# Optimization experiments

Measured on AMD Instinct MI355X. Metric: run time of the kernel, lower is better.

## Reference

```python
import jax, jax.numpy as jnp
import numpy as np
import math

# Config constants (match init_kwargs)
E = 8          # n_experts
TOPK = 2       # attn_topk
DIM = 1024     # transformer_dim
B = 4          # batch_size
S = 1024       # max_seq_len
H = 1024       # num_heads * head_dim
SCALE = 1.0 / math.sqrt(DIM)  # original divides scores by sqrt(self.dim)


def setup_inputs() -> dict:
    key = jax.random.key(0)
    ks = jax.random.split(key, 8)
    w = 0.02  # weight init scale
    return {
        "X": jax.random.normal(ks[0], (B, S, DIM), jnp.float32),
        "mask": jnp.ones((B, S), jnp.float32),
        "switch_W": jax.random.normal(ks[1], (DIM * S, E), jnp.float32) * w,
        "switch_b": jnp.zeros((E,), jnp.float32),
        "Wq": jax.random.normal(ks[2], (E, DIM, H), jnp.float32) * w,
        "bq": jnp.zeros((E, H), jnp.float32),
        "Wk": jax.random.normal(ks[3], (E, DIM, H), jnp.float32) * w,
        "bk": jnp.zeros((E, H), jnp.float32),
        "Wv": jax.random.normal(ks[4], (E, DIM, H), jnp.float32) * w,
        "bv": jnp.zeros((E, H), jnp.float32),
        "Wff": jax.random.normal(ks[5], (E, H, DIM), jnp.float32) * w,
        "bff": jnp.zeros((E, DIM), jnp.float32),
    }


def _dispatch_mask(route_prob):
    # top-k expert routing per batch element -> hard {0,1} mask [B, E]
    _, idx = jax.lax.top_k(route_prob, TOPK)  # [B, TOPK]
    b = route_prob.shape[0]
    return jnp.zeros((b, E), route_prob.dtype).at[jnp.arange(b)[:, None], idx].set(1.0)


def reference(X, mask, switch_W, switch_b, Wq, bq, Wk, bk, Wv, bv, Wff, bff):
    b, s, d = X.shape
    # Router: Linear(dim*seq_len -> n_experts) + softmax; preprocess -> idx_list
    logits = X.reshape(b, -1) @ switch_W + switch_b          # [B, E]
    route_prob = jax.nn.softmax(logits, axis=-1)
    m = _dispatch_mask(route_prob)                            # [B, E] dispatch mask (idx_list)

    # Per-expert Q/K/V projections (ColumnParallelLinearWithMoE over routed batches)
    Q = jnp.einsum('bsd,edh->ebsh', X, Wq) + bq[:, None, None, :]  # [E,B,S,H]
    K = jnp.einsum('bsd,edh->ebsh', X, Wk) + bk[:, None, None, :]
    V = jnp.einsum('bsd,edh->ebsh', X, Wv) + bv[:, None, None, :]

    # RowParallelMatmulWithMoE: per-expert scores, softmax (dropout p=0)
    scores = jnp.einsum('ebsh,ebth->ebst', Q, K) * SCALE      # [E,B,S,S]
    P = jax.nn.softmax(scores, axis=-1)

    # index_add_ combine of per-expert attn maps (second preprocess reuses same routing)
    A = jnp.einsum('be,ebst->bst', m, P)                      # [B,S,S]

    # ColumnParallelMatmulWithMoE: attn @ V per expert
    ctx = jnp.einsum('bst,ebth->ebsh', A, V)                  # [E,B,S,H]

    # RowParallelLinearWithMoE output projection, then index_add_ combine
    out = jnp.einsum('ebsh,ehd->ebsd', ctx, Wff) + bff[:, None, None, :]
    y = jnp.einsum('be,ebsd->bsd', m, out)                    # [B,S,DIM]
    return y
```

## Files before the change

### kernel.cpp

```cpp
#include <hip/hip_runtime.h>
#include <math.h>

typedef unsigned short u16;
typedef __attribute__((ext_vector_type(8))) short bffrag;
typedef __attribute__((ext_vector_type(4))) float f32x4;
typedef __attribute__((ext_vector_type(4))) unsigned short us4;
typedef __attribute__((ext_vector_type(8))) unsigned short us8;

#define SCALE_QK (1.0f/32.0f)

__device__ __forceinline__ u16 f2bf(float f) {
    unsigned u = __builtin_bit_cast(unsigned, f);
    u += 0x7fffu + ((u >> 16) & 1u);
    return (u16)(u >> 16);
}
__device__ __forceinline__ float bf2f(u16 v) {
    unsigned u = ((unsigned)v) << 16;
    return __builtin_bit_cast(float, u);
}

__device__ __forceinline__ void gld16(const u16* g, u16* l) {
    __builtin_amdgcn_global_load_lds(
        (const __attribute__((address_space(1))) void*)g,
        (__attribute__((address_space(3))) void*)l, 16, 0, 0);
}

__global__ __launch_bounds__(256) void router_partial(const float* __restrict__ X,
                                                      const float* __restrict__ sW,
                                                      float* __restrict__ part) {
    float acc[32];
    #pragma unroll
    for (int a = 0; a < 32; ++a) acc[a] = 0.f;
    int tid = blockIdx.x * 256 + threadIdx.x;
    #pragma unroll
    for (int q = 0; q < 4; ++q) {
        int i = tid + q * 262144;
        float4 w0 = *(const float4*)(sW + (size_t)i * 8);
        float4 w1 = *(const float4*)(sW + (size_t)i * 8 + 4);
        #pragma unroll
        for (int b = 0; b < 4; ++b) {
            float x = X[((size_t)b << 20) + i];
            acc[b*8+0] += x * w0.x; acc[b*8+1] += x * w0.y;
            acc[b*8+2] += x * w0.z; acc[b*8+3] += x * w0.w;
            acc[b*8+4] += x * w1.x; acc[b*8+5] += x * w1.y;
            acc[b*8+6] += x * w1.z; acc[b*8+7] += x * w1.w;
        }
    }
    __shared__ float wsum[4][32];
    int lane = threadIdx.x & 63, wv = threadIdx.x >> 6;
    #pragma unroll
    for (int a = 0; a < 32; ++a) {
        float v = acc[a];
        #pragma unroll
        for (int off = 32; off; off >>= 1) v += __shfl_down(v, off, 64);
        if (lane == 0) wsum[wv][a] = v;
    }
    __syncthreads();
    int t = threadIdx.x;
    if (t < 32)
        part[(size_t)t * 1024 + blockIdx.x] = wsum[0][t] + wsum[1][t] + wsum[2][t] + wsum[3][t];
}

__global__ __launch_bounds__(256) void router_final(const float* __restrict__ part,
                                                    const float* __restrict__ sb,
                                                    int* __restrict__ sel_need) {
    __shared__ float ps[32][8];
    __shared__ float lg[32];
    int t = threadIdx.x, a = t >> 3, c = t & 7;
    {
        float s = 0.f;
        const float* p = part + (size_t)a * 1024 + c * 128;
        for (int i = 0; i < 128; ++i) s += p[i];
        ps[a][c] = s;
    }
    __syncthreads();
    if (t < 32) {
        float v = 0.f;
        #pragma unroll
        for (int j = 0; j < 8; ++j) v += ps[t][j];
        lg[t] = v + sb[t & 7];
    }
    __syncthreads();
    if (t < 4) {
        int base = t * 8;
        int e1 = 0; float v1 = lg[base];
        for (int e = 1; e < 8; ++e) { if (lg[base + e] > v1) { v1 = lg[base + e]; e1 = e; } }
        int e2 = -1; float v2 = -INFINITY;
        for (int e = 0; e < 8; ++e) {
            if (e == e1) continue;
            if (lg[base + e] > v2) { v2 = lg[base + e]; e2 = e; }
        }
        sel_need[t * 2] = e1; sel_need[t * 2 + 1] = e2;
    }
    __syncthreads();
    if (t < 8) {
        int need = 0;
        for (int j = 0; j < 8; ++j) need |= (sel_need[j] == t);
        sel_need[8 + t] = need;
    }
}

__global__ __launch_bounds__(256) void cvt_all(const float* __restrict__ Wq,
                                               const float* __restrict__ Wk,
                                               const float* __restrict__ Wff,
                                               const float* __restrict__ X,
                                               const float* __restrict__ Wv,
                                               const float* __restrict__ bv,
                                               const int* __restrict__ sel_need,
                                               u16* __restrict__ WqT, u16* __restrict__ WkT,
                                               u16* __restrict__ WffT,
                                               u16* __restrict__ Xb, u16* __restrict__ WvB,
                                               float* __restrict__ cpart) {
    int z = blockIdx.z;
    int R0 = blockIdx.y * 128, C0 = blockIdx.x * 128;
    int t = threadIdx.x;
    if (z < 24) {
        int type = z >> 3, e = z & 7;
        if (!sel_need[8 + e]) return;
        const float* src = (type == 0 ? Wq : type == 1 ? Wk : Wff) + ((size_t)e << 20);
        u16* dst = (type == 0 ? WqT : type == 1 ? WkT : WffT) + ((size_t)e << 20);
        __shared__ u16 lt[128 * 136];
        int c = t & 127;
        int rh = (t >> 7) * 4;
        #pragma unroll
        for (int it = 0; it < 16; ++it) {
            int r4 = it * 8 + rh;
            us4 o;
            #pragma unroll
            for (int j = 0; j < 4; ++j)
                o[j] = f2bf(src[(size_t)(R0 + r4 + j) * 1024 + C0 + c]);
            *(us4*)&lt[c * 136 + r4] = o;
        }
        __syncthreads();
        int dd = (t & 15) * 8;
        int hh = t >> 4;
        #pragma unroll
        for (int it = 0; it < 8; ++it) {
            int cr = it * 16 + hh;
            us8 o = *(const us8*)&lt[cr * 136 + dd];
            *(us8*)(dst + (size_t)(C0 + cr) * 1024 + R0 + dd) = o;
        }
    } else if (z < 36) {
        const float* src; u16* dst;
        if (z < 28) {
            int b = z - 24;
            src = X + ((size_t)b << 20);  dst = Xb + ((size_t)b << 20);
        } else {
            int e = z - 28;
            if (!sel_need[8 + e]) return;
            src = Wv + ((size_t)e << 20);  dst = WvB + ((size_t)e << 20);
        }
        int r = t >> 4;
        int c8 = (t & 15) * 8;
        #pragma unroll
        for (int it = 0; it < 8; ++it) {
            int row = R0 + it * 16 + r;
            const float* sp = src + (size_t)row * 1024 + C0 + c8;
            float4 a = *(const float4*)sp;
            float4 b2 = *(const float4*)(sp + 4);
            us8 o;
            o[0] = f2bf(a.x); o[1] = f2bf(a.y); o[2] = f2bf(a.z); o[3] = f2bf(a.w);
            o[4] = f2bf(b2.x); o[5] = f2bf(b2.y); o[6] = f2bf(b2.z); o[7] = f2bf(b2.w);
            *(us8*)(dst + (size_t)row * 1024 + C0 + c8) = o;
        }
    } else {
        int idx = ((z - 36) << 6) + (blockIdx.y << 3) + blockIdx.x;
        int e = idx >> 5;
        if (!sel_need[8 + e]) return;
        int r = idx & 31;
        int d = (r & 3) * 256 + t;
        int h0 = (r >> 2) * 128;
        const float* W = Wff + ((size_t)e << 20) + (size_t)h0 * 1024 + d;
        const float* bvp = bv + e * 1024 + h0;
        float s = 0.f;
        #pragma unroll 4
        for (int h = 0; h < 128; ++h) s += bvp[h] * W[(size_t)h * 1024];
        cpart[(e * 8 + (r >> 2)) * 1024 + d] = s;
    }
}

__device__ __forceinline__ void stage_half8(const u16* g, int ld, u16* ldst, int tid) {
    int r = tid >> 3;
    int j = ((tid ^ r) & 7) * 8;
    gld16(g + (size_t)r * ld + j, ldst + tid * 8);
    gld16(g + (size_t)(r + 64) * ld + j, ldst + 4096 + tid * 8);
}

template<int Q, bool LASTVM>
__device__ __forceinline__ void phase8(const u16* Ac, const bffrag (&bfr)[4][2],
                                       f32x4 (&acc)[8][4], int rb, int l15, int x0,
                                       const u16* sg, int sld, u16* sdst, int tid) {
    bffrag af[2][2];
    #pragma unroll
    for (int mm = 0; mm < 2; ++mm) {
        int r = (rb + Q * 32 + mm * 16 + l15) * 64;
        af[mm][0] = *(const bffrag*)(Ac + r + x0);
        af[mm][1] = *(const bffrag*)(Ac + r + (x0 ^ 32));
    }
    __builtin_amdgcn_sched_barrier(0);
    stage_half8(sg, sld, sdst, tid);
    __builtin_amdgcn_sched_barrier(0);
    __builtin_amdgcn_s_barrier();
    asm volatile("s_waitcnt lgkmcnt(0)" ::: "memory");
    __builtin_amdgcn_sched_barrier(0);
    __builtin_amdgcn_s_setprio(1);
    #pragma unroll
    for (int ks = 0; ks < 2; ++ks)
        #pragma unroll
        for (int mm = 0; mm < 2; ++mm)
            #pragma unroll
            for (int nn = 0; nn < 4; ++nn)
                acc[Q*2+mm][nn] = __builtin_amdgcn_mfma_f32_16x16x32_bf16(
                    af[mm][ks], bfr[nn][ks], acc[Q*2+mm][nn], 0, 0, 0);
    __builtin_amdgcn_s_setprio(0);
    __builtin_amdgcn_sched_barrier(0);
    if (LASTVM) asm volatile("s_waitcnt vmcnt(4)" ::: "memory");
    __builtin_amdgcn_s_barrier();
}

__device__ __forceinline__ void gemm8(const u16* __restrict__ A, int lda,
                                      const u16* __restrict__ B, int ldb,
                                      int K, int m0, int n0, f32x4 (&acc)[8][4]) {
    __shared__ u16 lds[65536];
    const int tid = threadIdx.x, l = tid & 63, wid = tid >> 6;
    const int wr = wid >> 2, wc = wid & 3;
    const int l15 = l & 15;
    const int rb = wr * 128;
    const int cb = wc * 64;
    const int x0 = (((l >> 4) ^ (l & 7)) * 8);
    const int nt = K >> 6;

    const u16* Ag = A + (size_t)m0 * lda;
    const u16* Bg = B + (size_t)n0 * ldb;

    stage_half8(Ag,                          lda, lds,                 tid);
    stage_half8(Ag + (size_t)128 * lda,      lda, lds + 8192,          tid);
    stage_half8(Bg,                          ldb, lds + 16384,         tid);
    stage_half8(Bg + (size_t)128 * ldb,      ldb, lds + 16384 + 8192,  tid);
    stage_half8(Bg + 64,                     ldb, lds + 32768 + 16384, tid);
    stage_half8(Bg + 64 + (size_t)128 * ldb, ldb, lds + 32768 + 16384 + 8192, tid);
    asm volatile("s_waitcnt vmcnt(4)" ::: "memory");
    __builtin_amdgcn_s_barrier();

    for (int t7 = 0; t7 < nt; ++t7) {
        const int cur = t7 & 1;
        u16* Ac = lds + cur * 32768;
        u16* Bc = Ac + 16384;
        u16* An = lds + (cur ^ 1) * 32768;
        const int ka = (t7 + 1 < nt ? t7 + 1 : nt - 1) << 6;
        const int kb = (t7 + 2 < nt ? t7 + 2 : nt - 1) << 6;
        const u16* sA0 = Ag + ka;
        const u16* sA1 = Ag + (size_t)128 * lda + ka;
        const u16* sB0 = Bg + kb;
        const u16* sB1 = Bg + (size_t)128 * ldb + kb;

        bffrag bfr[4][2];
        #pragma unroll
        for (int nn = 0; nn < 4; ++nn) {
            int r = (cb + nn * 16 + l15) * 64;
            bfr[nn][0] = *(const bffrag*)(Bc + r + x0);
            bfr[nn][1] = *(const bffrag*)(Bc + r + (x0 ^ 32));
        }
        phase8<0, false>(Ac, bfr, acc, rb, l15, x0, sA0, lda, An, tid);
        phase8<1, false>(Ac, bfr, acc, rb, l15, x0, sA1, lda, An + 8192, tid);
        phase8<2, false>(Ac, bfr, acc, rb, l15, x0, sB0, ldb, Bc, tid);
        phase8<3, true >(Ac, bfr, acc, rb, l15, x0, sB1, ldb, Bc + 8192, tid);
    }
}

__device__ __forceinline__ void zero8(f32x4 (&acc)[8][4]) {
    #pragma unroll
    for (int m = 0; m < 8; ++m)
        #pragma unroll
        for (int n = 0; n < 4; ++n)
            #pragma unroll
            for (int i = 0; i < 4; ++i) acc[m][n][i] = 0.f;
}

__device__ __forceinline__ void epi8_bf16(u16* __restrict__ C, int ldc, float scale,
                                          const f32x4 (&acc)[8][4],
                                          const float* __restrict__ biasN,
                                          int M0, int N0) {
    const int tid = threadIdx.x, l = tid & 63, wid = tid >> 6;
    const int wr = wid >> 2, wc = wid & 3;
    const int m0 = M0 + wr * 128, n0 = N0 + wc * 64;
    const int l15 = l & 15, l4 = (l >> 4) * 4;
    #pragma unroll
    for (int mt = 0; mt < 8; ++mt)
        #pragma unroll
        for (int nn = 0; nn < 4; ++nn) {
            int col = n0 + nn * 16 + l15;
            float bn = biasN ? biasN[col] : 0.f;
            #pragma unroll
            for (int i = 0; i < 4; ++i) {
                int row = m0 + mt * 16 + l4 + i;
                C[(size_t)row * ldc + col] = f2bf(acc[mt][nn][i] * scale + bn);
            }
        }
}

__device__ __forceinline__ void xcd_decode(int f, int& z, int& m0, int& n0) {
    int xcd = f & 7, slot = f >> 3;
    z = xcd + ((slot >> 4) << 3);
    int idx = slot & 15;
    m0 = (idx >> 2) * 256;
    n0 = (idx & 3) * 256;
}

__global__ __launch_bounds__(512) void mfma8_qk(const u16* __restrict__ Xb,
        const u16* __restrict__ WqT, const u16* __restrict__ WkT,
        const float* __restrict__ bq, const float* __restrict__ bk,
        const int* __restrict__ sel, u16* __restrict__ Qb, u16* __restrict__ Kb) {
    int z, m0, n0;
    xcd_decode(blockIdx.x, z, m0, n0);
    int w = z >> 3, bs = z & 7;
    int b = bs >> 1, e = sel[bs];
    f32x4 acc[8][4]; zero8(acc);
    gemm8(Xb + ((size_t)b << 20), 1024, (w ? WkT : WqT) + ((size_t)e << 20), 1024,
          1024, m0, n0, acc);
    epi8_bf16((w ? Kb : Qb) + ((size_t)bs << 20), 1024, 1.0f, acc,
              (w ? bk : bq) + e * 1024, m0, n0);
}

__global__ __launch_bounds__(512) void mfma8_sw(const u16* __restrict__ Qb,
        const u16* __restrict__ Kb, const u16* __restrict__ WffT,
        const u16* __restrict__ WvB, const int* __restrict__ sel,
        u16* __restrict__ Sb, u16* __restrict__ P0b, u16* __restrict__ P1b) {
    int z, m0, n0;
    xcd_decode(blockIdx.x, z, m0, n0);
    f32x4 acc[8][4]; zero8(acc);
    if (z < 8) {
        gemm8(Qb + ((size_t)z << 20), 1024, Kb + ((size_t)z << 20), 1024, 1024, m0, n0, acc);
        epi8_bf16(Sb + ((size_t)z << 20), 1024, SCALE_QK, acc, nullptr, m0, n0);
    } else {
        int h = (z >= 12), b = z & 3, e = sel[b * 2 + h];
        gemm8(WffT + ((size_t)e << 20), 1024, WvB + ((size_t)e << 20), 1024, 1024, m0, n0, acc);
        epi8_bf16((h ? P1b : P0b) + ((size_t)b << 20), 1024, 1.0f, acc, nullptr, m0, n0);
    }
}

__global__ __launch_bounds__(256) void wvfadd(const u16* __restrict__ P0b,
                                              const u16* __restrict__ P1b,
                                              u16* __restrict__ W,
                                              const float* __restrict__ cpart,
                                              const float* __restrict__ bff,
                                              const int* __restrict__ sel,
                                              float* __restrict__ ybias) {
    int bid = blockIdx.x;
    if (bid >= 2048) {
        int r = bid - 2048;
        int b = r >> 2;
        int d = (r & 3) * 256 + threadIdx.x;
        int e0 = sel[b * 2], e1 = sel[b * 2 + 1];
        float c0 = 0.f, c1v = 0.f;
        #pragma unroll
        for (int hc = 0; hc < 8; ++hc) {
            c0  += cpart[(e0 * 8 + hc) * 1024 + d];
            c1v += cpart[(e1 * 8 + hc) * 1024 + d];
        }
        ybias[b * 1024 + d] = 2.f * (c0 + c1v) + bff[e0 * 1024 + d] + bff[e1 * 1024 + d];
        return;
    }
    size_t i = (size_t)(bid * 256 + threadIdx.x) * 8;
    us8 a = *(const us8*)(P0b + i);
    us8 b = *(const us8*)(P1b + i);
    us8 o;
    #pragma unroll
    for (int j = 0; j < 8; ++j) o[j] = f2bf(bf2f(a[j]) + bf2f(b[j]));
    *(us8*)(W + i) = o;
}

__device__ __forceinline__ void stage_tile(const u16* a0, const u16* a1,
                                           const u16* b0, const u16* b1,
                                           u16* sa, u16* sb, int tid) {
    gld16(a0, &sa[tid * 8]);
    gld16(a1, &sa[2048 + tid * 8]);
    gld16(b0, &sb[tid * 8]);
    gld16(b1, &sb[2048 + tid * 8]);
}

__device__ __forceinline__ void gemm_ds(const u16* __restrict__ A, int lda,
                                        const u16* __restrict__ B, int ldb,
                                        int K, int m0, int n0, f32x4 (&acc)[4][4]) {
    __shared__ u16 sA[2][4096];
    __shared__ u16 sB[2][4096];
    const int tid = threadIdx.x, lane = tid & 63, wv = tid >> 6;
    const int wr = (wv >> 1) * 64, wc = (wv & 1) * 64;
    const int l15 = lane & 15, lk = (lane >> 4) * 8;
    const int r0 = tid >> 2, k8 = (tid & 3) * 8;

    const u16* a0 = A + (size_t)(m0 + r0) * lda + k8;
    const u16* a1 = A + (size_t)(m0 + 64 + r0) * lda + k8;
    const u16* b0 = B + (size_t)(n0 + r0) * ldb + k8;
    const u16* b1 = B + (size_t)(n0 + 64 + r0) * ldb + k8;

    stage_tile(a0, a1, b0, b1, sA[0], sB[0], tid);
    __syncthreads();

    const int nt = K >> 5;
    for (int t = 0; t < nt; ++t) {
        const int cur = t & 1;
        if (t + 1 < nt) {
            int k0 = (t + 1) << 5;
            stage_tile(a0 + k0, a1 + k0, b0 + k0, b1 + k0, sA[cur ^ 1], sB[cur ^ 1], tid);
        }
        bffrag av[4], bf[4];
        #pragma unroll
        for (int m = 0; m < 4; ++m)
            av[m] = *reinterpret_cast<const bffrag*>(&sA[cur][(wr + m * 16 + l15) * 32 + lk]);
        #pragma unroll
        for (int n = 0; n < 4; ++n)
            bf[n] = *reinterpret_cast<const bffrag*>(&sB[cur][(wc + n * 16 + l15) * 32 + lk]);
        #pragma unroll
        for (int m = 0; m < 4; ++m)
            #pragma unroll
            for (int n = 0; n < 4; ++n)
                acc[m][n] = __builtin_amdgcn_mfma_f32_16x16x32_bf16(av[m], bf[n], acc[m][n], 0, 0, 0);
        __syncthreads();
    }
}

__device__ __forceinline__ void zero_acc(f32x4 (&acc)[4][4]) {
    #pragma unroll
    for (int m = 0; m < 4; ++m)
        #pragma unroll
        for (int n = 0; n < 4; ++n)
            #pragma unroll
            for (int i = 0; i < 4; ++i) acc[m][n][i] = 0.f;
}

__device__ __forceinline__ void epi4_bf16(u16* __restrict__ C, int ldc, int m0, int n0,
                                          const f32x4 (&acc)[4][4]) {
    const int tid = threadIdx.x, lane = tid & 63, wv = tid >> 6;
    const int wr = (wv >> 1) * 64, wc = (wv & 1) * 64;
    const int l15 = lane & 15, l4 = (lane >> 4) * 4;
    #pragma unroll
    for (int m = 0; m < 4; ++m)
        #pragma unroll
        for (int n = 0; n < 4; ++n) {
            int col = n0 + wc + n * 16 + l15;
            #pragma unroll
            for (int i = 0; i < 4; ++i) {
                int row = m0 + wr + m * 16 + l4 + i;
                C[(size_t)row * ldc + col] = f2bf(acc[m][n][i]);
            }
        }
}

__device__ __forceinline__ void epi4_f32(float* __restrict__ C, int ldc, int m0, int n0,
                                         const f32x4 (&acc)[4][4],
                                         const float* __restrict__ bias1) {
    const int tid = threadIdx.x, lane = tid & 63, wv = tid >> 6;
    const int wr = (wv >> 1) * 64, wc = (wv & 1) * 64;
    const int l15 = lane & 15, l4 = (lane >> 4) * 4;
    #pragma unroll
    for (int m = 0; m < 4; ++m)
        #pragma unroll
        for (int n = 0; n < 4; ++n) {
            int col = n0 + wc + n * 16 + l15;
            float bn = bias1 ? bias1[col] : 0.f;
            #pragma unroll
            for (int i = 0; i < 4; ++i) {
                int row = m0 + wr + m * 16 + l4 + i;
                C[(size_t)row * ldc + col] = acc[m][n][i] + bn;
            }
        }
}

__global__ __launch_bounds__(256) void sm_mt(const u16* __restrict__ Sb, u16* __restrict__ Ab,
        const u16* __restrict__ Wvfsum, const u16* __restrict__ Xb, u16* __restrict__ Mtb) {
    int bid = blockIdx.x;
    if (bid < 256) {
        int b = bid >> 6, m0 = ((bid >> 3) & 7) * 128, n0 = (bid & 7) * 128;
        f32x4 acc[4][4]; zero_acc(acc);
        gemm_ds(Wvfsum + ((size_t)b << 20), 1024, Xb + ((size_t)b << 20), 1024, 1024, m0, n0, acc);
        epi4_bf16(Mtb + ((size_t)b << 20), 1024, m0, n0, acc);
        return;
    }
    int bs = bid - 256, b = bs >> 10, s = bs & 1023;
    const u16* S0 = Sb + ((size_t)(b * 2) << 20) + (size_t)s * 1024;
    const u16* S1 = S0 + (1u << 20);
    int t = threadIdx.x, lane = t & 63, wv = t >> 6;
    us4 xv0 = *(const us4*)(S0 + t * 4);
    us4 xv1 = *(const us4*)(S1 + t * 4);
    float x0[4], x1[4];
    #pragma unroll
    for (int j = 0; j < 4; ++j) { x0[j] = bf2f(xv0[j]); x1[j] = bf2f(xv1[j]); }
    float m0 = fmaxf(fmaxf(x0[0], x0[1]), fmaxf(x0[2], x0[3]));
    float m1 = fmaxf(fmaxf(x1[0], x1[1]), fmaxf(x1[2], x1[3]));
    #pragma unroll
    for (int off = 32; off; off >>= 1) {
        m0 = fmaxf(m0, __shfl_xor(m0, off, 64));
        m1 = fmaxf(m1, __shfl_xor(m1, off, 64));
    }
    __shared__ float wred[4][4];
    if (lane == 0) { wred[wv][0] = m0; wred[wv][1] = m1; }
    __syncthreads();
    m0 = fmaxf(fmaxf(wred[0][0], wred[1][0]), fmaxf(wred[2][0], wred[3][0]));
    m1 = fmaxf(fmaxf(wred[0][1], wred[1][1]), fmaxf(wred[2][1], wred[3][1]));
    float e0[4], e1[4];
    #pragma unroll
    for (int j = 0; j < 4; ++j) { e0[j] = __expf(x0[j] - m0); e1[j] = __expf(x1[j] - m1); }
    float s0 = e0[0] + e0[1] + e0[2] + e0[3];
    float s1 = e1[0] + e1[1] + e1[2] + e1[3];
    #pragma unroll
    for (int off = 32; off; off >>= 1) {
        s0 += __shfl_xor(s0, off, 64);
        s1 += __shfl_xor(s1, off, 64);
    }
    if (lane == 0) { wred[wv][2] = s0; wred[wv][3] = s1; }
    __syncthreads();
    s0 = wred[0][2] + wred[1][2] + wred[2][2] + wred[3][2];
    s1 = wred[0][3] + wred[1][3] + wred[2][3] + wred[3][3];
    float r0 = 1.f / s0, r1 = 1.f / s1;
    us4 o;
    #pragma unroll
    for (int j = 0; j < 4; ++j) o[j] = f2bf(e0[j] * r0 + e1[j] * r1);
    *(us4*)(Ab + ((size_t)b << 20) + (size_t)s * 1024 + t * 4) = o;
}

__global__ __launch_bounds__(256) void mfma_y(const u16* __restrict__ Abf,
        const u16* __restrict__ Mtb, const float* __restrict__ ybias,
        float* __restrict__ y) {
    int b = blockIdx.z;
    int m0 = blockIdx.y * 128, n0 = blockIdx.x * 128;
    f32x4 acc[4][4]; zero_acc(acc);
    gemm_ds(Abf + ((size_t)b << 20), 1024, Mtb + ((size_t)b << 20), 1024, 1024, m0, n0, acc);
    epi4_f32(y + ((size_t)b << 20), 1024, m0, n0, acc, ybias + b * 1024);
}

extern "C" void kernel_launch(void* const* d_in, const int* in_sizes, int n_in,
                              void* d_out, int out_size, void* d_ws, size_t ws_size,
                              hipStream_t stream) {
    const float* X   = (const float*)d_in[0];
    const float* sW  = (const float*)d_in[2];
    const float* sb  = (const float*)d_in[3];
    const float* Wq  = (const float*)d_in[4];
    const float* bq  = (const float*)d_in[5];
    const float* Wk  = (const float*)d_in[6];
    const float* bk  = (const float*)d_in[7];
    const float* Wv  = (const float*)d_in[8];
    const float* bv  = (const float*)d_in[9];
    const float* Wff = (const float*)d_in[10];
    const float* bff = (const float*)d_in[11];
    float* y = (float*)d_out;

    char* w = (char*)d_ws;
    float* part  = (float*)w;
    float* cpart = (float*)w;
    int*   sel   = (int*)(w + (1u << 18));
    float* ybias = (float*)(w + (1u << 18) + 256);
    u16* base = (u16*)(w + (1u << 19));
    u16* Xb   = base;
    u16* WqT  = Xb   + (4u << 20);
    u16* WkT  = WqT  + (8u << 20);
    u16* WffT = WkT  + (8u << 20);
    u16* WvB  = WffT + (8u << 20);
    u16* Qb   = WvB  + (8u << 20);
    u16* Kb   = Qb   + (8u << 20);
    u16* Sb   = Kb   + (8u << 20);
    u16* P0b  = Sb   + (8u << 20);
    u16* P1b  = P0b  + (4u << 20);
    u16* Abf    = WqT;
    u16* Mtb    = WkT;
    u16* Wvfsum = Qb;

    router_partial<<<1024, 256, 0, stream>>>(X, sW, part);
    router_final<<<1, 256, 0, stream>>>(part, sb, sel);
    cvt_all<<<dim3(8, 8, 40), 256, 0, stream>>>(Wq, Wk, Wff, X, Wv, bv, sel,
                                                WqT, WkT, WffT, Xb, WvB, cpart);

    mfma8_qk<<<256, 512, 0, stream>>>(Xb, WqT, WkT, bq, bk, sel, Qb, Kb);
    mfma8_sw<<<256, 512, 0, stream>>>(Qb, Kb, WffT, WvB, sel, Sb, P0b, P1b);
    wvfadd<<<2064, 256, 0, stream>>>(P0b, P1b, Wvfsum, cpart, bff, sel, ybias);
    sm_mt<<<4352, 256, 0, stream>>>(Sb, Abf, Wvfsum, Xb, Mtb);
    mfma_y<<<dim3(8, 8, 4), 256, 0, stream>>>(Abf, Mtb, ybias, y);
}
```

Before: 204.3 us.

## Fuse X bf16 conversion into router and move bias-projection into wvfadd

The router kernel now writes the bf16 copy of X as it reads X, so the separate X conversion slices in cvt_all are dropped and X is read once instead of twice. The bv·Wff bias-projection partial sums are removed from cvt_all and computed directly in wvfadd's tail blocks from the transposed bf16 WffT, which shrinks the cvt_all grid. In exchange, each of the 16 tail blocks in wvfadd does a full 1024-long dot product per thread with strided row reads, and bf16 weights replace fp32 ones in that bias term. The router also gains scalar 2-byte stores.

```diff
diff --git a/kernel.cpp b/kernel.cpp
--- a/kernel.cpp
+++ b/kernel.cpp
@@ -27,7 +27,8 @@
 
 __global__ __launch_bounds__(256) void router_partial(const float* __restrict__ X,
                                                       const float* __restrict__ sW,
-                                                      float* __restrict__ part) {
+                                                      float* __restrict__ part,
+                                                      u16* __restrict__ Xb) {
     float acc[32];
     #pragma unroll
     for (int a = 0; a < 32; ++a) acc[a] = 0.f;
@@ -40,6 +41,7 @@
         #pragma unroll
         for (int b = 0; b < 4; ++b) {
             float x = X[((size_t)b << 20) + i];
+            Xb[((size_t)b << 20) + i] = f2bf(x);
             acc[b*8+0] += x * w0.x; acc[b*8+1] += x * w0.y;
             acc[b*8+2] += x * w0.z; acc[b*8+3] += x * w0.w;
             acc[b*8+4] += x * w1.x; acc[b*8+5] += x * w1.y;
@@ -103,14 +105,10 @@
 __global__ __launch_bounds__(256) void cvt_all(const float* __restrict__ Wq,
                                                const float* __restrict__ Wk,
                                                const float* __restrict__ Wff,
-                                               const float* __restrict__ X,
                                                const float* __restrict__ Wv,
-                                               const float* __restrict__ bv,
                                                const int* __restrict__ sel_need,
                                                u16* __restrict__ WqT, u16* __restrict__ WkT,
-                                               u16* __restrict__ WffT,
-                                               u16* __restrict__ Xb, u16* __restrict__ WvB,
-                                               float* __restrict__ cpart) {
+                                               u16* __restrict__ WffT, u16* __restrict__ WvB) {
     int z = blockIdx.z;
     int R0 = blockIdx.y * 128, C0 = blockIdx.x * 128;
     int t = threadIdx.x;
@@ -140,16 +138,11 @@
             us8 o = *(const us8*)&lt[cr * 136 + dd];
             *(us8*)(dst + (size_t)(C0 + cr) * 1024 + R0 + dd) = o;
         }
-    } else if (z < 36) {
-        const float* src; u16* dst;
-        if (z < 28) {
-            int b = z - 24;
-            src = X + ((size_t)b << 20);  dst = Xb + ((size_t)b << 20);
-        } else {
-            int e = z - 28;
-            if (!sel_need[8 + e]) return;
-            src = Wv + ((size_t)e << 20);  dst = WvB + ((size_t)e << 20);
-        }
+    } else {
+        int e = z - 24;
+        if (!sel_need[8 + e]) return;
+        const float* src = Wv + ((size_t)e << 20);
+        u16* dst = WvB + ((size_t)e << 20);
         int r = t >> 4;
         int c8 = (t & 15) * 8;
         #pragma unroll
@@ -163,19 +156,6 @@
             o[4] = f2bf(b2.x); o[5] = f2bf(b2.y); o[6] = f2bf(b2.z); o[7] = f2bf(b2.w);
             *(us8*)(dst + (size_t)row * 1024 + C0 + c8) = o;
         }
-    } else {
-        int idx = ((z - 36) << 6) + (blockIdx.y << 3) + blockIdx.x;
-        int e = idx >> 5;
-        if (!sel_need[8 + e]) return;
-        int r = idx & 31;
-        int d = (r & 3) * 256 + t;
-        int h0 = (r >> 2) * 128;
-        const float* W = Wff + ((size_t)e << 20) + (size_t)h0 * 1024 + d;
-        const float* bvp = bv + e * 1024 + h0;
-        float s = 0.f;
-        #pragma unroll 4
-        for (int h = 0; h < 128; ++h) s += bvp[h] * W[(size_t)h * 1024];
-        cpart[(e * 8 + (r >> 2)) * 1024 + d] = s;
     }
 }
 
@@ -342,23 +322,38 @@
 __global__ __launch_bounds__(256) void wvfadd(const u16* __restrict__ P0b,
                                               const u16* __restrict__ P1b,
                                               u16* __restrict__ W,
-                                              const float* __restrict__ cpart,
+                                              const u16* __restrict__ WffT,
+                                              const float* __restrict__ bv,
                                               const float* __restrict__ bff,
                                               const int* __restrict__ sel,
                                               float* __restrict__ ybias) {
     int bid = blockIdx.x;
     if (bid >= 2048) {
+        __shared__ float bv0[1024], bv1[1024];
         int r = bid - 2048;
         int b = r >> 2;
-        int d = (r & 3) * 256 + threadIdx.x;
+        int t = threadIdx.x;
+        int d2 = (r & 3) * 256 + t;
         int e0 = sel[b * 2], e1 = sel[b * 2 + 1];
+        #pragma unroll
+        for (int j = 0; j < 4; ++j) {
+            bv0[t + j * 256] = bv[e0 * 1024 + t + j * 256];
+            bv1[t + j * 256] = bv[e1 * 1024 + t + j * 256];
+        }
+        __syncthreads();
+        const u16* w0 = WffT + ((size_t)e0 << 20) + (size_t)d2 * 1024;
+        const u16* w1 = WffT + ((size_t)e1 << 20) + (size_t)d2 * 1024;
         float c0 = 0.f, c1v = 0.f;
-        #pragma unroll
-        for (int hc = 0; hc < 8; ++hc) {
-            c0  += cpart[(e0 * 8 + hc) * 1024 + d];
-            c1v += cpart[(e1 * 8 + hc) * 1024 + d];
-        }
-        ybias[b * 1024 + d] = 2.f * (c0 + c1v) + bff[e0 * 1024 + d] + bff[e1 * 1024 + d];
+        for (int h = 0; h < 1024; h += 8) {
+            us8 a = *(const us8*)(w0 + h);
+            us8 bb = *(const us8*)(w1 + h);
+            #pragma unroll
+            for (int j = 0; j < 8; ++j) {
+                c0  += bf2f(a[j])  * bv0[h + j];
+                c1v += bf2f(bb[j]) * bv1[h + j];
+            }
+        }
+        ybias[b * 1024 + d2] = 2.f * (c0 + c1v) + bff[e0 * 1024 + d2] + bff[e1 * 1024 + d2];
         return;
     }
     size_t i = (size_t)(bid * 256 + threadIdx.x) * 8;
@@ -547,7 +542,6 @@
 
     char* w = (char*)d_ws;
     float* part  = (float*)w;
-    float* cpart = (float*)w;
     int*   sel   = (int*)(w + (1u << 18));
     float* ybias = (float*)(w + (1u << 18) + 256);
     u16* base = (u16*)(w + (1u << 19));
@@ -565,14 +559,13 @@
     u16* Mtb    = WkT;
     u16* Wvfsum = Qb;
 
-    router_partial<<<1024, 256, 0, stream>>>(X, sW, part);
+    router_partial<<<1024, 256, 0, stream>>>(X, sW, part, Xb);
     router_final<<<1, 256, 0, stream>>>(part, sb, sel);
-    cvt_all<<<dim3(8, 8, 40), 256, 0, stream>>>(Wq, Wk, Wff, X, Wv, bv, sel,
-                                                WqT, WkT, WffT, Xb, WvB, cpart);
+    cvt_all<<<dim3(8, 8, 32), 256, 0, stream>>>(Wq, Wk, Wff, Wv, sel, WqT, WkT, WffT, WvB);
 
     mfma8_qk<<<256, 512, 0, stream>>>(Xb, WqT, WkT, bq, bk, sel, Qb, Kb);
     mfma8_sw<<<256, 512, 0, stream>>>(Qb, Kb, WffT, WvB, sel, Sb, P0b, P1b);
-    wvfadd<<<2064, 256, 0, stream>>>(P0b, P1b, Wvfsum, cpart, bff, sel, ybias);
+    wvfadd<<<2064, 256, 0, stream>>>(P0b, P1b, Wvfsum, WffT, bv, bff, sel, ybias);
     sm_mt<<<4352, 256, 0, stream>>>(Sb, Abf, Wvfsum, Xb, Mtb);
     mfma_y<<<dim3(8, 8, 4), 256, 0, stream>>>(Abf, Mtb, ybias, y);
 }
```

New measurement: 225.5 us. 10.4% more time.
